# Kernel optimization log

Measured on AMD Instinct MI355X. Metric: run time of the kernel, lower is better.

Reference implementation:

```python
import jax, jax.numpy as jnp
import numpy as np

B, S, D, M, O = 16, 1024, 1024, 1024, 1024


def _sq_cdist(x1, x2):
    # squared euclidean distance, shapes (..., n, d) x (..., m, d) -> (..., n, m)
    n1 = jnp.sum(x1 * x1, axis=-1, keepdims=True)            # (..., n, 1)
    n2 = jnp.sum(x2 * x2, axis=-1)[..., None, :]             # (..., 1, m)
    cross = jnp.einsum('...nd,...md->...nm', x1, x2)
    return jnp.maximum(n1 + n2 - 2.0 * cross, 0.0)


def _rbf(x1, x2, log_lengthscale):
    ls2 = jnp.exp(log_lengthscale) ** 2
    return jnp.exp(-0.5 * _sq_cdist(x1, x2) / ls2)


def setup_inputs() -> dict:
    key = jax.random.key(0)
    k1, k2, k3 = jax.random.split(key, 3)
    x = jax.random.normal(k1, (B, S, D), dtype=jnp.float32)
    inducing_points = jax.random.normal(k2, (M, D), dtype=jnp.float32)
    log_lengthscale = jnp.zeros((1,), dtype=jnp.float32)
    log_noise = jnp.zeros((1,), dtype=jnp.float32)
    # nn.Linear(n_inducing, output_dim).weight has shape (O, M)
    lim = 1.0 / np.sqrt(M)
    W_out = jax.random.uniform(k3, (O, M), minval=-lim, maxval=lim, dtype=jnp.float32)
    return {
        'x': x,
        'inducing_points': inducing_points,
        'log_lengthscale': log_lengthscale,
        'log_noise': log_noise,
        'W_out': W_out,
        'num_sentences': S,
    }


def reference(x, inducing_points, log_lengthscale, log_noise, W_out, num_sentences):
    ll = log_lengthscale[0]
    K_xx = _rbf(x, x, ll)                                    # (B, S, S)
    K_xi = _rbf(x, inducing_points[None], ll)                # (B, S, M)
    K_ii = _rbf(inducing_points, inducing_points, ll)        # (M, M)
    K_ii_reg = K_ii + jnp.exp(log_noise[0]) * jnp.eye(M, dtype=x.dtype)
    K_ii_inv = jnp.linalg.inv(K_ii_reg)                      # (M, M)
    A = jnp.einsum('bsm,mk->bsk', K_xi, K_ii_inv)            # (B, S, M)
    mean = jnp.einsum('bsm,om->bso', A, W_out)               # (B, S, O)
    var = K_xx - jnp.einsum('bsm,btm->bst', A, K_xi)         # (B, S, S)
    var_diag = jnp.diagonal(var, axis1=-2, axis2=-1)         # (B, S)
    var_out = jnp.broadcast_to(var_diag[..., None], (x.shape[0], num_sentences, W_out.shape[0]))
    return mean, jax.nn.softplus(var_out)
```

## Files before the change

kernel.cpp:

```cpp
#include <hip/hip_runtime.h>
#include <hip/hip_bf16.h>
#include <math.h>


typedef unsigned short u16;
typedef __attribute__((ext_vector_type(8))) short short8;
typedef __attribute__((ext_vector_type(4))) float f32x4;
typedef __attribute__((ext_vector_type(4))) unsigned short us4;

__device__ __forceinline__ float bf2f(u16 b) {
  union { unsigned u; float f; } x; x.u = ((unsigned)b) << 16; return x.f;
}
__device__ __forceinline__ u16 f2bf(float f) {
  union { float f; unsigned u; } x; x.f = f;
  unsigned r = x.u + 0x7fffu + ((x.u >> 16) & 1u);
  return (u16)(r >> 16);
}

__device__ __forceinline__ void gl_lds16(const void* g, void* l) {
  __builtin_amdgcn_global_load_lds(
      (const __attribute__((address_space(1))) void*)g,
      (__attribute__((address_space(3))) void*)l, 16, 0, 0);
}

template <int EPI>
__device__ __forceinline__ void big_body(
    int bid, u16* lds,
    const u16* Ag, const u16* Bg,
    float* outF, float* varF, u16* outB,
    const float* rowN, const float* colN,
    const float* p_ll, float* qb) {
  constexpr int NT = 16;
  const int tid = threadIdx.x;
  const int lane = tid & 63;
  const int wave = tid >> 6;
  const int wr = wave >> 1, wc = wave & 1;
  const int fro = lane & 15, khi = lane >> 4;
  const int xcd = bid & 7, j7 = bid >> 3;
  const size_t brow = (size_t)(xcd * 16 + (j7 >> 3));
  const size_t bcol = (size_t)(j7 & 7);

  if (EPI == 0) {
    if (tid < 16) qb[(size_t)bid * 16 + tid] = 0.0f;
  }

  f32x4 acc[4][4] = {};

  auto stageA = [&](int tt, int bb) {
#pragma unroll
    for (int c = 0; c < 4; ++c) {
      const int ci = tid + 256 * c;
      const int row = ci >> 3;
      const int gk = (ci & 7) ^ (row & 7);
      gl_lds16(Ag + (size_t)(brow * 128 + row) * 1024 + tt * 64 + gk * 8,
               &lds[bb * 16384 + ci * 8]);
    }
  };
  auto stageB = [&](int tt, int bb) {
#pragma unroll
    for (int c = 0; c < 4; ++c) {
      const int ci = tid + 256 * c;
      const int row = ci >> 3;
      const int gk = (ci & 7) ^ (row & 7);
      gl_lds16(Bg + (size_t)(bcol * 128 + row) * 1024 + tt * 64 + gk * 8,
               &lds[bb * 16384 + 8192 + ci * 8]);
    }
  };

  stageA(0, 0);
  stageB(0, 0);
  stageB(1, 1);
  asm volatile("s_waitcnt vmcnt(4)" ::: "memory");
  __builtin_amdgcn_s_barrier();

  for (int t = 0; t < NT; ++t) {
    const int cb = t & 1;
    const int ab = cb * 16384;
    const int bb = cb * 16384 + 8192;
    short8 bfrag[4][2];
#pragma unroll
    for (int p = 0; p < 4; ++p) {
      short8 afr[2];
      const int rr = wr * 64 + p * 16 + fro;
#pragma unroll
      for (int s = 0; s < 2; ++s) {
        const int kl = (s * 4 + khi) ^ (rr & 7);
        afr[s] = *(const short8*)&lds[ab + (rr * 8 + kl) * 8];
      }
      if (p == 0) {
#pragma unroll
        for (int n = 0; n < 4; ++n) {
          const int cc = wc * 64 + n * 16 + fro;
#pragma unroll
          for (int s = 0; s < 2; ++s) {
            const int kl = (s * 4 + khi) ^ (cc & 7);
            bfrag[n][s] = *(const short8*)&lds[bb + (cc * 8 + kl) * 8];
          }
        }
        if (t + 1 < NT) stageA(t + 1, cb ^ 1);
      } else if (p == 1) {
        if (t + 2 < NT) stageB(t + 2, cb);
      }
      __builtin_amdgcn_s_setprio(1);
#pragma unroll
      for (int n = 0; n < 4; ++n)
#pragma unroll
        for (int s = 0; s < 2; ++s)
          acc[p][n] = __builtin_amdgcn_mfma_f32_16x16x32_bf16(
              afr[s], bfrag[n][s], acc[p][n], 0, 0, 0);
      __builtin_amdgcn_s_setprio(0);
      if (p == 3) {
        if (t < NT - 2) asm volatile("s_waitcnt vmcnt(4)" ::: "memory");
        else            asm volatile("s_waitcnt vmcnt(0)" ::: "memory");
      }
      __builtin_amdgcn_s_barrier();
    }
  }

  float inv2 = 0.f;
  if (EPI == 0) inv2 = 0.5f * expf(-2.0f * p_ll[0]);
#pragma unroll
  for (int m = 0; m < 4; m++) {
#pragma unroll
    for (int j = 0; j < 4; j++) {
      const size_t grow = brow * 128 + wr * 64 + m * 16 + khi * 4 + j;
      float rn = 0.f, sp = 0.f;
      if (EPI == 0) rn = rowN[grow];
      if (EPI == 1) {
        float vq = 1.0f - qb[grow];
        sp = fmaxf(vq, 0.f) + log1pf(expf(-fabsf(vq)));
      }
      float part = 0.f;
#pragma unroll
      for (int n = 0; n < 4; n++) {
        const size_t gcol = bcol * 128 + wc * 64 + n * 16 + fro;
        const size_t o = grow * 1024 + gcol;
        float v = acc[m][n][j];
        if (EPI == 0) {
          float d2 = fmaxf(rn + colN[gcol] - 2.0f * v, 0.0f);
          outB[o] = f2bf(expf(-inv2 * d2));
        } else if (EPI == 1) {
          outF[o] = v;
          varF[o] = sp;
        } else {
          part += v * v;
        }
      }
      if (EPI == 2) {
        part += __shfl_xor(part, 1);
        part += __shfl_xor(part, 2);
        part += __shfl_xor(part, 4);
        part += __shfl_xor(part, 8);
        if (fro == 0) atomicAdd(&qb[grow], part);
      }
    }
  }
}

__device__ __forceinline__ void small_core(const u16* Ap, const u16* Bp,
                                           u16* As, u16* Bs,
                                           f32x4 (&acc)[4][4]) {
  const int tid = threadIdx.x;
  const int lane = tid & 63;
  const int wave = tid >> 6;
  const int wr = wave >> 1, wc = wave & 1;
  const int idx0 = tid, idx1 = tid + 256;
  const u16* gA0 = Ap + (size_t)(idx0 >> 2) * 1024 + (size_t)(idx0 & 3) * 8;
  const u16* gA1 = Ap + (size_t)(idx1 >> 2) * 1024 + (size_t)(idx1 & 3) * 8;
  const u16* gB0 = Bp + (size_t)(idx0 >> 2) * 1024 + (size_t)(idx0 & 3) * 8;
  const u16* gB1 = Bp + (size_t)(idx1 >> 2) * 1024 + (size_t)(idx1 & 3) * 8;
  u16* lA0 = &As[idx0 * 8]; u16* lA1 = &As[idx1 * 8];
  u16* lB0 = &Bs[idx0 * 8]; u16* lB1 = &Bs[idx1 * 8];
  const int fro = lane & 15;
  const int ko = (lane >> 4) * 8;

  for (int kt = 0; kt < 1024; kt += 32) {
    gl_lds16(gA0 + kt, lA0);
    gl_lds16(gA1 + kt, lA1);
    gl_lds16(gB0 + kt, lB0);
    gl_lds16(gB1 + kt, lB1);
    __syncthreads();
    short8 af[4], bfr[4];
#pragma unroll
    for (int m = 0; m < 4; m++) {
      af[m]  = *(const short8*)&As[(wr * 64 + m * 16 + fro) * 32 + ko];
      bfr[m] = *(const short8*)&Bs[(wc * 64 + m * 16 + fro) * 32 + ko];
    }
#pragma unroll
    for (int m = 0; m < 4; m++)
#pragma unroll
      for (int n = 0; n < 4; n++)
        acc[m][n] = __builtin_amdgcn_mfma_f32_16x16x32_bf16(af[m], bfr[n], acc[m][n], 0, 0, 0);
    __syncthreads();
  }
}

__device__ __forceinline__ void kii_body(int bid, u16* lds,
                                         const u16* ipb, u16* kii,
                                         const float* ni, const float* ll,
                                         const float* ln, float* rs) {
  const int by = bid >> 3, bx = bid & 7;
  f32x4 acc[4][4] = {};
  small_core(ipb + (size_t)by * 131072, ipb + (size_t)bx * 131072,
             lds, lds + 4096, acc);
  const int lane = threadIdx.x & 63;
  const int wave = threadIdx.x >> 6;
  const int wr = wave >> 1, wc = wave & 1;
  float inv2 = 0.5f * expf(-2.0f * ll[0]);
  float noise = expf(ln[0]);
#pragma unroll
  for (int m = 0; m < 4; m++)
#pragma unroll
    for (int j = 0; j < 4; j++) {
      const size_t grow = by * 128 + wr * 64 + m * 16 + (lane >> 4) * 4 + j;
      float rn = ni[grow];
      float part = 0.f;
#pragma unroll
      for (int n = 0; n < 4; n++) {
        const size_t gcol = bx * 128 + wc * 64 + n * 16 + (lane & 15);
        float d2 = fmaxf(rn + ni[gcol] - 2.0f * acc[m][n][j], 0.0f);
        float kv = (grow == gcol) ? (1.0f + noise) : expf(-inv2 * d2);
        kii[grow * 1024 + gcol] = f2bf(kv);
        part += fabsf(kv);
      }
      part += __shfl_xor(part, 1);
      part += __shfl_xor(part, 2);
      part += __shfl_xor(part, 4);
      part += __shfl_xor(part, 8);
      if ((lane & 15) == 0) atomicAdd(&rs[grow], part);
    }
}

__device__ __forceinline__ void batch1_body(int bid, u16* lds,
                                            const u16* kii, const u16* Wb,
                                            u16* R2b, u16* T1b,
                                            const float* sc) {
  const int z = bid >> 6, r = bid & 63;
  const int by = r >> 3, bx = r & 7;
  f32x4 acc[4][4] = {};
  const u16* Abase = z ? Wb : kii;
  small_core(Abase + (size_t)by * 131072, kii + (size_t)bx * 131072,
             lds, lds + 4096, acc);
  const int lane = threadIdx.x & 63;
  const int wave = threadIdx.x >> 6;
  const int wr = wave >> 1, wc = wave & 1;
  const float c = sc[0];
#pragma unroll
  for (int m = 0; m < 4; m++)
#pragma unroll
    for (int j = 0; j < 4; j++) {
      const size_t grow = by * 128 + wr * 64 + m * 16 + (lane >> 4) * 4 + j;
#pragma unroll
      for (int n = 0; n < 4; n++) {
        const size_t gcol = bx * 128 + wc * 64 + n * 16 + (lane & 15);
        const size_t o = grow * 1024 + gcol;
        float v = acc[m][n][j];
        if (z == 0) {
          float idv = (grow == gcol) ? 1.0f : 0.0f;
          R2b[o] = f2bf(idv - 2.0f * c * bf2f(kii[o]) + c * c * v);
        } else {
          T1b[o] = f2bf(2.0f * bf2f(Wb[o]) - c * v);
        }
      }
    }
}

__device__ __forceinline__ void batch2_body(int z, int by, int bx, u16* lds,
                                            const u16* kii, const u16* R2b,
                                            const u16* T1b, u16* U,
                                            const float* sc) {
  f32x4 acc[4][4] = {};
  const u16* Abase = z ? T1b : kii;
  small_core(Abase + (size_t)by * 131072, R2b + (size_t)bx * 131072,
             lds, lds + 4096, acc);
  const int lane = threadIdx.x & 63;
  const int wave = threadIdx.x >> 6;
  const int wr = wave >> 1, wc = wave & 1;
  const float c = sc[0], s = sc[1];
#pragma unroll
  for (int m = 0; m < 4; m++)
#pragma unroll
    for (int j = 0; j < 4; j++) {
      const size_t grow = by * 128 + wr * 64 + m * 16 + (lane >> 4) * 4 + j;
#pragma unroll
      for (int n = 0; n < 4; n++) {
        const size_t gcol = bx * 128 + wc * 64 + n * 16 + (lane & 15);
        const size_t o = grow * 1024 + gcol;
        float v = acc[m][n][j];
        if (z == 0) {
          float idv = (grow == gcol) ? 1.0f : 0.0f;
          U[o] = f2bf(s * (1.5f * idv - 0.5f * c * bf2f(kii[o]) +
                           0.6875f * bf2f(R2b[o]) - 0.3125f * c * v));
        } else {
          U[o + 1048576] = f2bf(c * (bf2f(T1b[o]) + v));
        }
      }
    }
}

__device__ __forceinline__ void prepx_body(int bid, u16* lds,
                                           const float* x, u16* xbf,
                                           float* nx) {
  float* wsum = (float*)lds;
  for (int r = bid; r < 16384; r += 2048) {
    const float4 v = ((const float4*)(x + (size_t)r * 1024))[threadIdx.x];
    float ss = v.x * v.x + v.y * v.y + v.z * v.z + v.w * v.w;
    us4 o; o.x = f2bf(v.x); o.y = f2bf(v.y); o.z = f2bf(v.z); o.w = f2bf(v.w);
    ((us4*)(xbf + (size_t)r * 1024))[threadIdx.x] = o;
#pragma unroll
    for (int s = 32; s > 0; s >>= 1) ss += __shfl_xor(ss, s);
    if ((threadIdx.x & 63) == 0) wsum[threadIdx.x >> 6] = ss;
    __syncthreads();
    if (threadIdx.x == 0) nx[r] = wsum[0] + wsum[1] + wsum[2] + wsum[3];
    __syncthreads();
  }
}

__global__ __launch_bounds__(256) void fat1(
    const float* __restrict__ x, u16* __restrict__ xbf, float* __restrict__ nx,
    const u16* __restrict__ ipb, u16* __restrict__ kii,
    const float* __restrict__ ni, const float* __restrict__ ll,
    const float* __restrict__ ln, float* __restrict__ rs) {
  __shared__ u16 lds[8192];
  const int bid = blockIdx.x;
  if (bid < 64) kii_body(bid, lds, ipb, kii, ni, ll, ln, rs);
  else          prepx_body(bid - 64, lds, x, xbf, nx);
}

__global__ __launch_bounds__(256, 2) void fat2(
    const u16* __restrict__ xbf, const u16* __restrict__ ipb,
    u16* __restrict__ kxib,
    const float* __restrict__ nx, const float* __restrict__ ni,
    const float* __restrict__ ll, float* __restrict__ qb,
    const u16* __restrict__ kii, const u16* __restrict__ wbf,
    u16* __restrict__ R2b, u16* __restrict__ t1b,
    const float* __restrict__ sc) {
  __shared__ u16 lds[32768];
  const int bid = blockIdx.x;
  if (bid < 128) batch1_body(bid, lds, kii, wbf, R2b, t1b, sc);
  else big_body<0>(bid - 128, lds, xbf, ipb, nullptr, nullptr, kxib,
                   nx, ni, ll, qb);
}

__global__ __launch_bounds__(256) void kbatch2a(
    const u16* __restrict__ kii, const u16* __restrict__ R2b,
    const u16* __restrict__ t1b, u16* __restrict__ U,
    const float* __restrict__ sc) {
  __shared__ u16 lds[8192];
  batch2_body(0, blockIdx.y, blockIdx.x, lds, kii, R2b, t1b, U, sc);
}

__global__ __launch_bounds__(256, 2) void fat3(
    const u16* __restrict__ kxib, const u16* __restrict__ U,
    float* __restrict__ qb,
    const u16* __restrict__ kii, const u16* __restrict__ R2b,
    const u16* __restrict__ t1b, u16* __restrict__ Uw,
    const float* __restrict__ sc) {
  __shared__ u16 lds[32768];
  const int bid = blockIdx.x;
  if (bid < 64) batch2_body(1, bid >> 3, bid & 7, lds, kii, R2b, t1b, Uw, sc);
  else big_body<2>(bid - 64, lds, kxib, U, nullptr, nullptr, nullptr,
                   nullptr, nullptr, nullptr, qb);
}

__global__ __launch_bounds__(256, 2) void kmean(
    const u16* __restrict__ kxib, const u16* __restrict__ w2t,
    float* __restrict__ meanO, float* __restrict__ varO,
    float* __restrict__ qb) {
  __shared__ u16 lds[32768];
  big_body<1>(blockIdx.x, lds, kxib, w2t, meanO, varO, nullptr,
              nullptr, nullptr, nullptr, qb);
}

__global__ __launch_bounds__(256) void prep_ipw(const float* __restrict__ ip,
                                                const float* __restrict__ W,
                                                u16* __restrict__ ipb,
                                                u16* __restrict__ wbf,
                                                float* __restrict__ ni,
                                                float* __restrict__ rs) {
  __shared__ float wsum[4];
  int b = blockIdx.x;
  if (b < 1024) {
    const float4 v = ((const float4*)(ip + (size_t)b * 1024))[threadIdx.x];
    float ss = v.x * v.x + v.y * v.y + v.z * v.z + v.w * v.w;
    us4 o; o.x = f2bf(v.x); o.y = f2bf(v.y); o.z = f2bf(v.z); o.w = f2bf(v.w);
    ((us4*)(ipb + (size_t)b * 1024))[threadIdx.x] = o;
#pragma unroll
    for (int s = 32; s > 0; s >>= 1) ss += __shfl_xor(ss, s);
    if ((threadIdx.x & 63) == 0) wsum[threadIdx.x >> 6] = ss;
    __syncthreads();
    if (threadIdx.x == 0) {
      ni[b] = wsum[0] + wsum[1] + wsum[2] + wsum[3];
      rs[b] = 0.0f;
    }
  } else {
    int r = b - 1024;
    const float4 v = ((const float4*)(W + (size_t)r * 1024))[threadIdx.x];
    us4 o; o.x = f2bf(v.x); o.y = f2bf(v.y); o.z = f2bf(v.z); o.w = f2bf(v.w);
    ((us4*)(wbf + (size_t)r * 1024))[threadIdx.x] = o;
  }
}

__global__ __launch_bounds__(256) void gmax_inv(const float* __restrict__ rs,
                                                float* __restrict__ sc) {
  __shared__ float wm[4];
  float m = 0.f;
  for (int i = threadIdx.x; i < 1024; i += 256) m = fmaxf(m, rs[i]);
#pragma unroll
  for (int o = 32; o > 0; o >>= 1) m = fmaxf(m, __shfl_xor(m, o));
  if ((threadIdx.x & 63) == 0) wm[threadIdx.x >> 6] = m;
  __syncthreads();
  if (threadIdx.x == 0) {
    float c = 1.0f / fmaxf(fmaxf(wm[0], wm[1]), fmaxf(wm[2], wm[3]));
    sc[0] = c;
    sc[1] = sqrtf(c);
  }
}

extern "C" void kernel_launch(void* const* d_in, const int* in_sizes, int n_in,
                              void* d_out, int out_size, void* d_ws, size_t ws_size,
                              hipStream_t stream) {
  const float* x  = (const float*)d_in[0];
  const float* ip = (const float*)d_in[1];
  const float* ll = (const float*)d_in[2];
  const float* ln = (const float*)d_in[3];
  const float* W  = (const float*)d_in[4];

  char* ws = (char*)d_ws;
  const size_t MB = 1ull << 20;
  u16* kxib = (u16*)(ws + 0 * MB);
  u16* xbf  = (u16*)(ws + 32 * MB);
  u16* ipb  = (u16*)(ws + 64 * MB);
  u16* wbf  = (u16*)(ws + 66 * MB);
  u16* kii  = (u16*)(ws + 68 * MB);
  u16* R2b  = (u16*)(ws + 70 * MB);
  u16* Ub   = (u16*)(ws + 74 * MB);
  u16* t1b  = (u16*)(ws + 78 * MB);
  float* nx = (float*)(ws + 80 * MB);
  float* qb = (float*)(ws + 80 * MB + 128 * 1024);
  float* ni = (float*)(ws + 80 * MB + 256 * 1024);
  float* rs = (float*)(ws + 80 * MB + 512 * 1024);
  float* sc = (float*)(ws + 80 * MB + 768 * 1024);

  float* meanO = (float*)d_out;
  float* varO  = meanO + 16777216ull;

  prep_ipw<<<2048, 256, 0, stream>>>(ip, W, ipb, wbf, ni, rs);

  fat1<<<2112, 256, 0, stream>>>(x, xbf, nx, ipb, kii, ni, ll, ln, rs);

  gmax_inv<<<1, 256, 0, stream>>>(rs, sc);

  fat2<<<1152, 256, 0, stream>>>(xbf, ipb, kxib, nx, ni, ll, qb,
                                 kii, wbf, R2b, t1b, sc);

  kbatch2a<<<dim3(8, 8), 256, 0, stream>>>(kii, R2b, t1b, Ub, sc);

  fat3<<<1088, 256, 0, stream>>>(kxib, Ub, qb, kii, R2b, t1b, Ub, sc);

  kmean<<<1024, 256, 0, stream>>>(kxib, Ub + 1048576, meanO, varO, qb);
}
```

Before: 212.6 us.

## Fuse variance and mean GEMMs into one launch with last-block softplus epilogue

```diff
diff --git a/kernel.cpp b/kernel.cpp
--- a/kernel.cpp
+++ b/kernel.cpp
@@ -29,7 +29,7 @@
     const u16* Ag, const u16* Bg,
     float* outF, float* varF, u16* outB,
     const float* rowN, const float* colN,
-    const float* p_ll, float* qb) {
+    const float* p_ll, float* qb, unsigned* tick) {
   constexpr int NT = 16;
   const int tid = threadIdx.x;
   const int lane = tid & 63;
@@ -42,6 +42,7 @@
 
   if (EPI == 0) {
     if (tid < 16) qb[(size_t)bid * 16 + tid] = 0.0f;
+    if (tid == 16 && bid < 128) tick[bid] = 0u;
   }
 
   f32x4 acc[4][4] = {};
@@ -124,12 +125,8 @@
 #pragma unroll
     for (int j = 0; j < 4; j++) {
       const size_t grow = brow * 128 + wr * 64 + m * 16 + khi * 4 + j;
-      float rn = 0.f, sp = 0.f;
+      float rn = 0.f;
       if (EPI == 0) rn = rowN[grow];
-      if (EPI == 1) {
-        float vq = 1.0f - qb[grow];
-        sp = fmaxf(vq, 0.f) + log1pf(expf(-fabsf(vq)));
-      }
       float part = 0.f;
 #pragma unroll
       for (int n = 0; n < 4; n++) {
@@ -141,7 +138,6 @@
           outB[o] = f2bf(expf(-inv2 * d2));
         } else if (EPI == 1) {
           outF[o] = v;
-          varF[o] = sp;
         } else {
           part += v * v;
         }
@@ -152,6 +148,27 @@
         part += __shfl_xor(part, 4);
         part += __shfl_xor(part, 8);
         if (fro == 0) atomicAdd(&qb[grow], part);
+      }
+    }
+  }
+
+  if (EPI == 2) {
+    __syncthreads();
+    __threadfence();
+    volatile unsigned* lastp = (volatile unsigned*)lds;
+    if (tid == 0) lastp[0] = (atomicAdd(&tick[brow], 1u) == 7u) ? 1u : 0u;
+    __syncthreads();
+    if (lastp[0]) {
+      __threadfence();
+      for (int r = wave; r < 128; r += 4) {
+        float qv = __hip_atomic_load(&qb[brow * 128 + r], __ATOMIC_RELAXED,
+                                     __HIP_MEMORY_SCOPE_AGENT);
+        float vq = 1.0f - qv;
+        float sp = fmaxf(vq, 0.f) + log1pf(expf(-fabsf(vq)));
+        float4 o4 = {sp, sp, sp, sp};
+        float4* dst = (float4*)(varF + (size_t)(brow * 128 + r) * 1024);
+#pragma unroll
+        for (int cc = lane; cc < 256; cc += 64) dst[cc] = o4;
       }
     }
   }
@@ -332,6 +349,7 @@
     u16* __restrict__ kxib,
     const float* __restrict__ nx, const float* __restrict__ ni,
     const float* __restrict__ ll, float* __restrict__ qb,
+    unsigned* __restrict__ tick,
     const u16* __restrict__ kii, const u16* __restrict__ wbf,
     u16* __restrict__ R2b, u16* __restrict__ t1b,
     const float* __restrict__ sc) {
@@ -339,37 +357,32 @@
   const int bid = blockIdx.x;
   if (bid < 128) batch1_body(bid, lds, kii, wbf, R2b, t1b, sc);
   else big_body<0>(bid - 128, lds, xbf, ipb, nullptr, nullptr, kxib,
-                   nx, ni, ll, qb);
-}
-
-__global__ __launch_bounds__(256) void kbatch2a(
+                   nx, ni, ll, qb, tick);
+}
+
+__global__ __launch_bounds__(256) void kbatch2(
     const u16* __restrict__ kii, const u16* __restrict__ R2b,
     const u16* __restrict__ t1b, u16* __restrict__ U,
     const float* __restrict__ sc) {
   __shared__ u16 lds[8192];
-  batch2_body(0, blockIdx.y, blockIdx.x, lds, kii, R2b, t1b, U, sc);
-}
-
-__global__ __launch_bounds__(256, 2) void fat3(
+  const int bid = blockIdx.x;
+  const int z = bid >> 6, r = bid & 63;
+  batch2_body(z, r >> 3, r & 7, lds, kii, R2b, t1b, U, sc);
+}
+
+__global__ __launch_bounds__(256, 2) void fatqm(
     const u16* __restrict__ kxib, const u16* __restrict__ U,
-    float* __restrict__ qb,
-    const u16* __restrict__ kii, const u16* __restrict__ R2b,
-    const u16* __restrict__ t1b, u16* __restrict__ Uw,
-    const float* __restrict__ sc) {
+    const u16* __restrict__ w2t,
+    float* __restrict__ meanO, float* __restrict__ varO,
+    float* __restrict__ qb, unsigned* __restrict__ tick) {
   __shared__ u16 lds[32768];
   const int bid = blockIdx.x;
-  if (bid < 64) batch2_body(1, bid >> 3, bid & 7, lds, kii, R2b, t1b, Uw, sc);
-  else big_body<2>(bid - 64, lds, kxib, U, nullptr, nullptr, nullptr,
-                   nullptr, nullptr, nullptr, qb);
-}
-
-__global__ __launch_bounds__(256, 2) void kmean(
-    const u16* __restrict__ kxib, const u16* __restrict__ w2t,
-    float* __restrict__ meanO, float* __restrict__ varO,
-    float* __restrict__ qb) {
-  __shared__ u16 lds[32768];
-  big_body<1>(blockIdx.x, lds, kxib, w2t, meanO, varO, nullptr,
-              nullptr, nullptr, nullptr, qb);
+  if (bid < 1024)
+    big_body<2>(bid, lds, kxib, U, nullptr, varO, nullptr,
+                nullptr, nullptr, nullptr, qb, tick);
+  else
+    big_body<1>(bid - 1024, lds, kxib, w2t, meanO, nullptr, nullptr,
+                nullptr, nullptr, nullptr, qb, tick);
 }
 
 __global__ __launch_bounds__(256) void prep_ipw(const float* __restrict__ ip,
@@ -441,6 +454,7 @@
   float* ni = (float*)(ws + 80 * MB + 256 * 1024);
   float* rs = (float*)(ws + 80 * MB + 512 * 1024);
   float* sc = (float*)(ws + 80 * MB + 768 * 1024);
+  unsigned* tick = (unsigned*)(ws + 80 * MB + 1024 * 1024);
 
   float* meanO = (float*)d_out;
   float* varO  = meanO + 16777216ull;
@@ -451,12 +465,11 @@
 
   gmax_inv<<<1, 256, 0, stream>>>(rs, sc);
 
-  fat2<<<1152, 256, 0, stream>>>(xbf, ipb, kxib, nx, ni, ll, qb,
+  fat2<<<1152, 256, 0, stream>>>(xbf, ipb, kxib, nx, ni, ll, qb, tick,
                                  kii, wbf, R2b, t1b, sc);
 
-  kbatch2a<<<dim3(8, 8), 256, 0, stream>>>(kii, R2b, t1b, Ub, sc);
-
-  fat3<<<1088, 256, 0, stream>>>(kxib, Ub, qb, kii, R2b, t1b, Ub, sc);
-
-  kmean<<<1024, 256, 0, stream>>>(kxib, Ub + 1048576, meanO, varO, qb);
-}
+  kbatch2<<<128, 256, 0, stream>>>(kii, R2b, t1b, Ub, sc);
+
+  fatqm<<<2048, 256, 0, stream>>>(kxib, Ub, Ub + 1048576, meanO, varO,
+                                  qb, tick);
+}
```

New measurement: 327.9 us. 1.54x slower.

## Fold scale reduction into consumer blocks and move Kii·R2 GEMM onto pipelined body

Applied to the files above, without the earlier changes.

```diff
diff --git a/kernel.cpp b/kernel.cpp
--- a/kernel.cpp
+++ b/kernel.cpp
@@ -21,6 +21,17 @@
   __builtin_amdgcn_global_load_lds(
       (const __attribute__((address_space(1))) void*)g,
       (__attribute__((address_space(3))) void*)l, 16, 0, 0);
+}
+
+__device__ __forceinline__ float local_cmax(const float* rs, float* sm) {
+  float m = 0.f;
+  for (int i = threadIdx.x; i < 1024; i += 256) m = fmaxf(m, rs[i]);
+#pragma unroll
+  for (int o = 32; o > 0; o >>= 1) m = fmaxf(m, __shfl_xor(m, o));
+  __syncthreads();
+  if ((threadIdx.x & 63) == 0) sm[threadIdx.x >> 6] = m;
+  __syncthreads();
+  return 1.0f / fmaxf(fmaxf(sm[0], sm[1]), fmaxf(sm[2], sm[3]));
 }
 
 template <int EPI>
@@ -36,9 +47,15 @@
   const int wave = tid >> 6;
   const int wr = wave >> 1, wc = wave & 1;
   const int fro = lane & 15, khi = lane >> 4;
-  const int xcd = bid & 7, j7 = bid >> 3;
-  const size_t brow = (size_t)(xcd * 16 + (j7 >> 3));
-  const size_t bcol = (size_t)(j7 & 7);
+  size_t brow, bcol;
+  if (EPI == 3) {
+    brow = (size_t)(bid >> 3);
+    bcol = (size_t)(bid & 7);
+  } else {
+    const int xcd = bid & 7, j7 = bid >> 3;
+    brow = (size_t)(xcd * 16 + (j7 >> 3));
+    bcol = (size_t)(j7 & 7);
+  }
 
   if (EPI == 0) {
     if (tid < 16) qb[(size_t)bid * 16 + tid] = 0.0f;
@@ -117,8 +134,13 @@
     }
   }
 
-  float inv2 = 0.f;
+  float inv2 = 0.f, cc2 = 0.f, ss2 = 0.f;
   if (EPI == 0) inv2 = 0.5f * expf(-2.0f * p_ll[0]);
+  if (EPI == 3) {
+    __syncthreads();
+    cc2 = local_cmax(rowN, (float*)lds);
+    ss2 = sqrtf(cc2);
+  }
 #pragma unroll
   for (int m = 0; m < 4; m++) {
 #pragma unroll
@@ -142,6 +164,10 @@
         } else if (EPI == 1) {
           outF[o] = v;
           varF[o] = sp;
+        } else if (EPI == 3) {
+          float idv = (grow == gcol) ? 1.0f : 0.0f;
+          outB[o] = f2bf(ss2 * (1.5f * idv - 0.5f * cc2 * bf2f(Ag[o]) +
+                                0.6875f * bf2f(Bg[o]) - 0.3125f * cc2 * v));
         } else {
           part += v * v;
         }
@@ -234,17 +260,18 @@
 __device__ __forceinline__ void batch1_body(int bid, u16* lds,
                                             const u16* kii, const u16* Wb,
                                             u16* R2b, u16* T1b,
-                                            const float* sc) {
+                                            const float* rs) {
   const int z = bid >> 6, r = bid & 63;
   const int by = r >> 3, bx = r & 7;
   f32x4 acc[4][4] = {};
   const u16* Abase = z ? Wb : kii;
   small_core(Abase + (size_t)by * 131072, kii + (size_t)bx * 131072,
              lds, lds + 4096, acc);
+  __syncthreads();
+  const float c = local_cmax(rs, (float*)lds);
   const int lane = threadIdx.x & 63;
   const int wave = threadIdx.x >> 6;
   const int wr = wave >> 1, wc = wave & 1;
-  const float c = sc[0];
 #pragma unroll
   for (int m = 0; m < 4; m++)
 #pragma unroll
@@ -265,18 +292,17 @@
     }
 }
 
-__device__ __forceinline__ void batch2_body(int z, int by, int bx, u16* lds,
-                                            const u16* kii, const u16* R2b,
-                                            const u16* T1b, u16* U,
-                                            const float* sc) {
+__device__ __forceinline__ void batch2b_body(int by, int bx, u16* lds,
+                                             const u16* R2b, const u16* T1b,
+                                             u16* U, const float* rs) {
   f32x4 acc[4][4] = {};
-  const u16* Abase = z ? T1b : kii;
-  small_core(Abase + (size_t)by * 131072, R2b + (size_t)bx * 131072,
+  small_core(T1b + (size_t)by * 131072, R2b + (size_t)bx * 131072,
              lds, lds + 4096, acc);
+  __syncthreads();
+  const float c = local_cmax(rs, (float*)lds);
   const int lane = threadIdx.x & 63;
   const int wave = threadIdx.x >> 6;
   const int wr = wave >> 1, wc = wave & 1;
-  const float c = sc[0], s = sc[1];
 #pragma unroll
   for (int m = 0; m < 4; m++)
 #pragma unroll
@@ -286,14 +312,7 @@
       for (int n = 0; n < 4; n++) {
         const size_t gcol = bx * 128 + wc * 64 + n * 16 + (lane & 15);
         const size_t o = grow * 1024 + gcol;
-        float v = acc[m][n][j];
-        if (z == 0) {
-          float idv = (grow == gcol) ? 1.0f : 0.0f;
-          U[o] = f2bf(s * (1.5f * idv - 0.5f * c * bf2f(kii[o]) +
-                           0.6875f * bf2f(R2b[o]) - 0.3125f * c * v));
-        } else {
-          U[o + 1048576] = f2bf(c * (bf2f(T1b[o]) + v));
-        }
+        U[o + 1048576] = f2bf(c * (bf2f(T1b[o]) + acc[m][n][j]));
       }
     }
 }
@@ -334,31 +353,30 @@
     const float* __restrict__ ll, float* __restrict__ qb,
     const u16* __restrict__ kii, const u16* __restrict__ wbf,
     u16* __restrict__ R2b, u16* __restrict__ t1b,
-    const float* __restrict__ sc) {
+    const float* __restrict__ rs) {
   __shared__ u16 lds[32768];
   const int bid = blockIdx.x;
-  if (bid < 128) batch1_body(bid, lds, kii, wbf, R2b, t1b, sc);
+  if (bid < 128) batch1_body(bid, lds, kii, wbf, R2b, t1b, rs);
   else big_body<0>(bid - 128, lds, xbf, ipb, nullptr, nullptr, kxib,
                    nx, ni, ll, qb);
 }
 
-__global__ __launch_bounds__(256) void kbatch2a(
+__global__ __launch_bounds__(256, 2) void gemm_s(
     const u16* __restrict__ kii, const u16* __restrict__ R2b,
-    const u16* __restrict__ t1b, u16* __restrict__ U,
-    const float* __restrict__ sc) {
-  __shared__ u16 lds[8192];
-  batch2_body(0, blockIdx.y, blockIdx.x, lds, kii, R2b, t1b, U, sc);
+    u16* __restrict__ U, const float* __restrict__ rs) {
+  __shared__ u16 lds[32768];
+  big_body<3>(blockIdx.x, lds, kii, R2b, nullptr, nullptr, U,
+              rs, nullptr, nullptr, nullptr);
 }
 
 __global__ __launch_bounds__(256, 2) void fat3(
     const u16* __restrict__ kxib, const u16* __restrict__ U,
     float* __restrict__ qb,
-    const u16* __restrict__ kii, const u16* __restrict__ R2b,
-    const u16* __restrict__ t1b, u16* __restrict__ Uw,
-    const float* __restrict__ sc) {
+    const u16* __restrict__ R2b, const u16* __restrict__ t1b,
+    u16* __restrict__ Uw, const float* __restrict__ rs) {
   __shared__ u16 lds[32768];
   const int bid = blockIdx.x;
-  if (bid < 64) batch2_body(1, bid >> 3, bid & 7, lds, kii, R2b, t1b, Uw, sc);
+  if (bid < 64) batch2b_body(bid >> 3, bid & 7, lds, R2b, t1b, Uw, rs);
   else big_body<2>(bid - 64, lds, kxib, U, nullptr, nullptr, nullptr,
                    nullptr, nullptr, nullptr, qb);
 }
@@ -398,22 +416,6 @@
     const float4 v = ((const float4*)(W + (size_t)r * 1024))[threadIdx.x];
     us4 o; o.x = f2bf(v.x); o.y = f2bf(v.y); o.z = f2bf(v.z); o.w = f2bf(v.w);
     ((us4*)(wbf + (size_t)r * 1024))[threadIdx.x] = o;
-  }
-}
-
-__global__ __launch_bounds__(256) void gmax_inv(const float* __restrict__ rs,
-                                                float* __restrict__ sc) {
-  __shared__ float wm[4];
-  float m = 0.f;
-  for (int i = threadIdx.x; i < 1024; i += 256) m = fmaxf(m, rs[i]);
-#pragma unroll
-  for (int o = 32; o > 0; o >>= 1) m = fmaxf(m, __shfl_xor(m, o));
-  if ((threadIdx.x & 63) == 0) wm[threadIdx.x >> 6] = m;
-  __syncthreads();
-  if (threadIdx.x == 0) {
-    float c = 1.0f / fmaxf(fmaxf(wm[0], wm[1]), fmaxf(wm[2], wm[3]));
-    sc[0] = c;
-    sc[1] = sqrtf(c);
   }
 }
 
@@ -440,7 +442,6 @@
   float* qb = (float*)(ws + 80 * MB + 128 * 1024);
   float* ni = (float*)(ws + 80 * MB + 256 * 1024);
   float* rs = (float*)(ws + 80 * MB + 512 * 1024);
-  float* sc = (float*)(ws + 80 * MB + 768 * 1024);
 
   float* meanO = (float*)d_out;
   float* varO  = meanO + 16777216ull;
@@ -449,14 +450,12 @@
 
   fat1<<<2112, 256, 0, stream>>>(x, xbf, nx, ipb, kii, ni, ll, ln, rs);
 
-  gmax_inv<<<1, 256, 0, stream>>>(rs, sc);
-
   fat2<<<1152, 256, 0, stream>>>(xbf, ipb, kxib, nx, ni, ll, qb,
-                                 kii, wbf, R2b, t1b, sc);
-
-  kbatch2a<<<dim3(8, 8), 256, 0, stream>>>(kii, R2b, t1b, Ub, sc);
-
-  fat3<<<1088, 256, 0, stream>>>(kxib, Ub, qb, kii, R2b, t1b, Ub, sc);
+                                 kii, wbf, R2b, t1b, rs);
+
+  gemm_s<<<64, 256, 0, stream>>>(kii, R2b, Ub, rs);
+
+  fat3<<<1088, 256, 0, stream>>>(kxib, Ub, qb, R2b, t1b, Ub, rs);
 
   kmean<<<1024, 256, 0, stream>>>(kxib, Ub + 1048576, meanO, varO, qb);
 }
```

After: 203.1 us, median of 2. 4.5% less time.
